# Performance work log

Hardware: AMD Instinct MI355X
Metric: run time of the kernel (lower is better)

The kernel has to match this reference:

```python
import jax, jax.numpy as jnp
import numpy as np

BATCH = 4096
DIM = 2048
TEMP = 0.5
EPS = 1e-12  # matches F.normalize eps


def setup_inputs() -> dict:
    key = jax.random.key(0)
    k1, k2 = jax.random.split(key)
    x_i = jax.random.normal(k1, (BATCH, DIM), dtype=jnp.float32)
    x_j = jax.random.normal(k2, (BATCH, DIM), dtype=jnp.float32)
    return {"x_i": x_i, "x_j": x_j}


def _l2_normalize(x):
    # F.normalize(x, dim=1): x / max(||x||, eps)
    n = jnp.sqrt(jnp.sum(x * x, axis=1, keepdims=True))
    return x / jnp.maximum(n, EPS)


def reference(x_i, x_j):
    N = x_i.shape[0]
    z = jnp.concatenate([_l2_normalize(x_i), _l2_normalize(x_j)], axis=0)  # (2N, D)
    # cosine sim of unit vectors == dot product -> single GEMM instead of (2N,2N,D) broadcast
    sim = z @ z.T  # (2N, 2N)
    # positives: diag offset +N and -N
    sim_ij = jnp.diagonal(sim, offset=N)
    sim_ji = jnp.diagonal(sim, offset=-N)
    pos = jnp.concatenate([sim_ij, sim_ji], axis=0)  # (2N,)
    nom = jnp.exp(pos / TEMP)
    neg_mask = 1.0 - jnp.eye(2 * N, dtype=sim.dtype)
    denom = jnp.sum(neg_mask * jnp.exp(sim / TEMP), axis=1)  # (2N,)
    return jnp.sum(-jnp.log(nom / denom)) / (2 * N)
```

## Files before the change

### kernel.cpp

```cpp
#include <hip/hip_runtime.h>
#include <hip/hip_bf16.h>

#define N_ROWS 8192
#define N_HALF 4096
#define DIM    2048
#define ROWB   2048
#define INV_T  2.0f
#define QSCL   64.0f
#define SIMSCL 0.00048828125f
#define NG1    1024
#define NG2    256
#define NKT    32

typedef __attribute__((ext_vector_type(4))) float f32x4;
typedef __attribute__((ext_vector_type(2))) long lx2;

__device__ __forceinline__ void gload_lds16(const void* g, void* l) {
  __builtin_amdgcn_global_load_lds(
      (const __attribute__((address_space(1))) unsigned int*)g,
      (__attribute__((address_space(3))) unsigned int*)l, 16, 0, 0);
}

__global__ __launch_bounds__(256) void normpos_k(
    const float* __restrict__ xi, const float* __restrict__ xj,
    char* __restrict__ zq, float* __restrict__ pos,
    float* __restrict__ selfd, float* __restrict__ denom)
{
  const int b = blockIdx.x;
  const int t = threadIdx.x;
  const float4* si = (const float4*)(xi + (size_t)b * DIM);
  const float4* sj = (const float4*)(xj + (size_t)b * DIM);
  float4 a0 = si[t * 2], a1 = si[t * 2 + 1];
  float4 c0 = sj[t * 2], c1 = sj[t * 2 + 1];
  float ssi = a0.x*a0.x + a0.y*a0.y + a0.z*a0.z + a0.w*a0.w
            + a1.x*a1.x + a1.y*a1.y + a1.z*a1.z + a1.w*a1.w;
  float ssj = c0.x*c0.x + c0.y*c0.y + c0.z*c0.z + c0.w*c0.w
            + c1.x*c1.x + c1.y*c1.y + c1.z*c1.z + c1.w*c1.w;
  #pragma unroll
  for (int m = 1; m < 64; m <<= 1) {
    ssi += __shfl_xor(ssi, m, 64);
    ssj += __shfl_xor(ssj, m, 64);
  }
  __shared__ float ri[4], rj[4];
  if ((t & 63) == 0) { ri[t >> 6] = ssi; rj[t >> 6] = ssj; }
  __syncthreads();
  float sci = 1.0f / fmaxf(sqrtf(ri[0] + ri[1] + ri[2] + ri[3]), 1e-12f);
  float scj = 1.0f / fmaxf(sqrtf(rj[0] + rj[1] + rj[2] + rj[3]), 1e-12f);

  float fi[8] = {a0.x, a0.y, a0.z, a0.w, a1.x, a1.y, a1.z, a1.w};
  float fj[8] = {c0.x, c0.y, c0.z, c0.w, c1.x, c1.y, c1.z, c1.w};
  float ni[8], nj[8];
  float dp = 0.f;
  #pragma unroll
  for (int e = 0; e < 8; ++e) {
    ni[e] = fi[e] * sci;
    nj[e] = fj[e] * scj;
    dp += ni[e] * nj[e];
  }
  int wi0 = 0, wi1 = 0, wj0 = 0, wj1 = 0;
  wi0 = __builtin_amdgcn_cvt_pk_fp8_f32(ni[0]*QSCL, ni[1]*QSCL, wi0, false);
  wi0 = __builtin_amdgcn_cvt_pk_fp8_f32(ni[2]*QSCL, ni[3]*QSCL, wi0, true);
  wi1 = __builtin_amdgcn_cvt_pk_fp8_f32(ni[4]*QSCL, ni[5]*QSCL, wi1, false);
  wi1 = __builtin_amdgcn_cvt_pk_fp8_f32(ni[6]*QSCL, ni[7]*QSCL, wi1, true);
  wj0 = __builtin_amdgcn_cvt_pk_fp8_f32(nj[0]*QSCL, nj[1]*QSCL, wj0, false);
  wj0 = __builtin_amdgcn_cvt_pk_fp8_f32(nj[2]*QSCL, nj[3]*QSCL, wj0, true);
  wj1 = __builtin_amdgcn_cvt_pk_fp8_f32(nj[4]*QSCL, nj[5]*QSCL, wj1, false);
  wj1 = __builtin_amdgcn_cvt_pk_fp8_f32(nj[6]*QSCL, nj[7]*QSCL, wj1, true);

  const size_t ipos = (size_t)(t >> 3) * 64 + (t & 3) * 16 + ((t >> 2) & 1) * 8;
  *(int2*)(zq + (size_t)b * ROWB + ipos)            = make_int2(wi0, wi1);
  *(int2*)(zq + (size_t)(b + N_HALF) * ROWB + ipos) = make_int2(wj0, wj1);

  float dsi = 0.f, dsj = 0.f;
  {
    float d;
    d = __builtin_amdgcn_cvt_f32_fp8(wi0, 0); dsi += d * d;
    d = __builtin_amdgcn_cvt_f32_fp8(wi0, 1); dsi += d * d;
    d = __builtin_amdgcn_cvt_f32_fp8(wi0, 2); dsi += d * d;
    d = __builtin_amdgcn_cvt_f32_fp8(wi0, 3); dsi += d * d;
    d = __builtin_amdgcn_cvt_f32_fp8(wi1, 0); dsi += d * d;
    d = __builtin_amdgcn_cvt_f32_fp8(wi1, 1); dsi += d * d;
    d = __builtin_amdgcn_cvt_f32_fp8(wi1, 2); dsi += d * d;
    d = __builtin_amdgcn_cvt_f32_fp8(wi1, 3); dsi += d * d;
    d = __builtin_amdgcn_cvt_f32_fp8(wj0, 0); dsj += d * d;
    d = __builtin_amdgcn_cvt_f32_fp8(wj0, 1); dsj += d * d;
    d = __builtin_amdgcn_cvt_f32_fp8(wj0, 2); dsj += d * d;
    d = __builtin_amdgcn_cvt_f32_fp8(wj0, 3); dsj += d * d;
    d = __builtin_amdgcn_cvt_f32_fp8(wj1, 0); dsj += d * d;
    d = __builtin_amdgcn_cvt_f32_fp8(wj1, 1); dsj += d * d;
    d = __builtin_amdgcn_cvt_f32_fp8(wj1, 2); dsj += d * d;
    d = __builtin_amdgcn_cvt_f32_fp8(wj1, 3); dsj += d * d;
  }
  #pragma unroll
  for (int m = 1; m < 64; m <<= 1) {
    dp  += __shfl_xor(dp, m, 64);
    dsi += __shfl_xor(dsi, m, 64);
    dsj += __shfl_xor(dsj, m, 64);
  }
  __shared__ float rp[4], rsi[4], rsj[4];
  if ((t & 63) == 0) { rp[t >> 6] = dp; rsi[t >> 6] = dsi; rsj[t >> 6] = dsj; }
  __syncthreads();
  if (t == 0) {
    float p = rp[0] + rp[1] + rp[2] + rp[3];
    pos[b]            = p;
    pos[b + N_HALF]   = p;
    selfd[b]          = rsi[0] + rsi[1] + rsi[2] + rsi[3];
    selfd[b + N_HALF] = rsj[0] + rsj[1] + rsj[2] + rsj[3];
    denom[b]          = 0.f;
    denom[b + N_HALF] = 0.f;
  }
}

__global__ __launch_bounds__(512, 4) void simexp_k(
    const char* __restrict__ zq, float* __restrict__ denom)
{
  __shared__ char lds[73728];
  char* ldsA = lds;
  char* ldsB = lds + 49152;

  const int t    = threadIdx.x;
  const int wave = t >> 6, lane = t & 63;
  const int o    = lane >> 4;
  const int bid  = blockIdx.x;

  const int sqq = t >> 3;
  const int s0  = (t & 7) ^ (sqq & 7);
  const int srr = s0 >> 2;
  const int so  = s0 & 3;

  if (bid < NG1) {
    const int wr = wave >> 1, wc = wave & 1;

    int rem = (bid & 7) * (NG1 / 8) + (bid >> 3);
    int bi = 0;
    while (rem >= 63 - 2 * bi) { rem -= 63 - 2 * bi; ++bi; }
    const int bj   = 2 * bi + rem;
    const int row0 = bi * 256;
    const int col0 = bj * 128;

    const char* srcA0 = zq + (size_t)(row0 + 2 * sqq + srr) * ROWB + so * 16;
    const char* srcA1 = srcA0 + (size_t)128 * ROWB;
    const char* srcB  = zq + (size_t)(col0 + 2 * sqq + srr) * ROWB + so * 16;
    char* dA = ldsA + wave * 1024;
    char* dB = ldsB + wave * 1024;

    int offA[4], offB[4];
    #pragma unroll
    for (int m = 0; m < 4; ++m) {
      int r = wr * 64 + m * 16 + (lane & 15);
      int q = r >> 1;
      offA[m] = q * 128 + ((((r & 1) * 4 + o) ^ (q & 7)) << 4);
    }
    #pragma unroll
    for (int n = 0; n < 4; ++n) {
      int r = wc * 64 + n * 16 + (lane & 15);
      int q = r >> 1;
      offB[n] = q * 128 + ((((r & 1) * 4 + o) ^ (q & 7)) << 4);
    }

    f32x4 acc[4][4] = {};

#define STAGE(kt, slot) do {                                   \
      gload_lds16(srcA0 + (kt) * 64, dA + (slot) * 16384);     \
      gload_lds16(srcA1 + (kt) * 64, dA + (slot) * 16384 + 8192); \
      gload_lds16(srcB  + (kt) * 64, dB + (slot) * 8192);      \
    } while (0)

    STAGE(0, 0);
    STAGE(1, 1);

    int sl = 0;
    for (int p = 0; p < NKT; ++p) {
      if (p < NKT - 1) asm volatile("s_waitcnt vmcnt(3)" ::: "memory");
      else             asm volatile("s_waitcnt vmcnt(0)" ::: "memory");
      __builtin_amdgcn_s_barrier();
      __builtin_amdgcn_sched_barrier(0);

      const char* Ab = ldsA + sl * 16384;
      const char* Bb = ldsB + sl * 8192;
      lx2 a[4], b[4];
      #pragma unroll
      for (int m = 0; m < 4; ++m) a[m] = *(const lx2*)(Ab + offA[m]);
      #pragma unroll
      for (int n = 0; n < 4; ++n) b[n] = *(const lx2*)(Bb + offB[n]);

      if (p + 2 < NKT) {
        int s2 = sl + 2; if (s2 >= 3) s2 -= 3;
        STAGE(p + 2, s2);
      }

      __builtin_amdgcn_s_setprio(1);
      #pragma unroll
      for (int m = 0; m < 4; ++m)
        #pragma unroll
        for (int n = 0; n < 4; ++n)
          acc[m][n] = __builtin_amdgcn_mfma_f32_16x16x32_fp8_fp8(
              a[m][0], b[n][0], acc[m][n], 0, 0, 0);
      #pragma unroll
      for (int m = 0; m < 4; ++m)
        #pragma unroll
        for (int n = 0; n < 4; ++n)
          acc[m][n] = __builtin_amdgcn_mfma_f32_16x16x32_fp8_fp8(
              a[m][1], b[n][1], acc[m][n], 0, 0, 0);
      __builtin_amdgcn_s_setprio(0);
      __builtin_amdgcn_sched_barrier(0);

      if (++sl >= 3) sl = 0;
    }
#undef STAGE

    #pragma unroll
    for (int m = 0; m < 4; ++m)
      #pragma unroll
      for (int n = 0; n < 4; ++n)
        #pragma unroll
        for (int r = 0; r < 4; ++r)
          acc[m][n][r] = __expf(acc[m][n][r] * SIMSCL);

    #pragma unroll
    for (int m = 0; m < 4; ++m) {
      #pragma unroll
      for (int r = 0; r < 4; ++r) {
        float s = acc[m][0][r] + acc[m][1][r] + acc[m][2][r] + acc[m][3][r];
        s += __shfl_xor(s, 1, 64);
        s += __shfl_xor(s, 2, 64);
        s += __shfl_xor(s, 4, 64);
        s += __shfl_xor(s, 8, 64);
        if ((lane & 15) == 0) {
          int grow = row0 + wr * 64 + m * 16 + (lane >> 4) * 4 + r;
          atomicAdd(&denom[grow], s);
        }
      }
    }

    if (bj >= 2 * bi + 2) {
      #pragma unroll
      for (int n = 0; n < 4; ++n) {
        float cs = 0.f;
        #pragma unroll
        for (int m = 0; m < 4; ++m)
          #pragma unroll
          for (int r = 0; r < 4; ++r)
            cs += acc[m][n][r];
        cs += __shfl_xor(cs, 16, 64);
        cs += __shfl_xor(cs, 32, 64);
        if ((lane >> 4) == 0) {
          int gcol = col0 + wc * 64 + n * 16 + (lane & 15);
          atomicAdd(&denom[gcol], cs);
        }
      }
    }
  } else {
    const int sub  = bid - NG1;
    const int bi   = sub >> 3;
    const int row0 = bi * 256 + (sub & 7) * 32;
    const int col0 = 8064;

    const char* srcB = zq + (size_t)(col0 + 2 * sqq + srr) * ROWB + so * 16;
    const int tA   = t & 127;
    const int sqA  = tA >> 3;
    const int s0A  = (tA & 7) ^ (sqA & 7);
    const char* srcAs = zq + (size_t)(row0 + 2 * sqA + (s0A >> 2)) * ROWB
                      + (s0A & 3) * 16;

    int offA2[2], offB0;
    #pragma unroll
    for (int m = 0; m < 2; ++m) {
      int r = m * 16 + (lane & 15);
      int q = r >> 1;
      offA2[m] = q * 128 + ((((r & 1) * 4 + o) ^ (q & 7)) << 4);
    }
    {
      int r = wave * 16 + (lane & 15);
      int q = r >> 1;
      offB0 = q * 128 + ((((r & 1) * 4 + o) ^ (q & 7)) << 4);
    }

    f32x4 acc2[2] = {};

#define STAGE_T(kt, slot) do {                                            \
      gload_lds16(srcB + (kt) * 64, ldsB + (slot) * 8192 + wave * 1024);  \
      if (wave < 2)                                                       \
        gload_lds16(srcAs + (kt) * 64,                                    \
                    ldsA + (slot) * 2048 + wave * 1024);                  \
    } while (0)

    STAGE_T(0, 0);
    STAGE_T(1, 1);

    int sl = 0;
    for (int p = 0; p < NKT; ++p) {
      if (p < NKT - 1) {
        if (wave < 2) asm volatile("s_waitcnt vmcnt(2)" ::: "memory");
        else          asm volatile("s_waitcnt vmcnt(1)" ::: "memory");
      } else {
        asm volatile("s_waitcnt vmcnt(0)" ::: "memory");
      }
      __builtin_amdgcn_s_barrier();
      __builtin_amdgcn_sched_barrier(0);

      const char* Ab = ldsA + sl * 2048;
      const char* Bb = ldsB + sl * 8192;
      lx2 a0 = *(const lx2*)(Ab + offA2[0]);
      lx2 a1 = *(const lx2*)(Ab + offA2[1]);
      lx2 b0 = *(const lx2*)(Bb + offB0);

      if (p + 2 < NKT) {
        int s2 = sl + 2; if (s2 >= 3) s2 -= 3;
        STAGE_T(p + 2, s2);
      }

      __builtin_amdgcn_s_setprio(1);
      acc2[0] = __builtin_amdgcn_mfma_f32_16x16x32_fp8_fp8(a0[0], b0[0], acc2[0], 0, 0, 0);
      acc2[1] = __builtin_amdgcn_mfma_f32_16x16x32_fp8_fp8(a1[0], b0[0], acc2[1], 0, 0, 0);
      acc2[0] = __builtin_amdgcn_mfma_f32_16x16x32_fp8_fp8(a0[1], b0[1], acc2[0], 0, 0, 0);
      acc2[1] = __builtin_amdgcn_mfma_f32_16x16x32_fp8_fp8(a1[1], b0[1], acc2[1], 0, 0, 0);
      __builtin_amdgcn_s_setprio(0);
      __builtin_amdgcn_sched_barrier(0);

      if (++sl >= 3) sl = 0;
    }
#undef STAGE_T

    #pragma unroll
    for (int m = 0; m < 2; ++m)
      #pragma unroll
      for (int r = 0; r < 4; ++r)
        acc2[m][r] = __expf(acc2[m][r] * SIMSCL);

    #pragma unroll
    for (int m = 0; m < 2; ++m) {
      #pragma unroll
      for (int r = 0; r < 4; ++r) {
        float s = acc2[m][r];
        s += __shfl_xor(s, 1, 64);
        s += __shfl_xor(s, 2, 64);
        s += __shfl_xor(s, 4, 64);
        s += __shfl_xor(s, 8, 64);
        if ((lane & 15) == 0) {
          int grow = row0 + m * 16 + (lane >> 4) * 4 + r;
          atomicAdd(&denom[grow], s);
        }
      }
    }

    if (bi <= 30) {
      float cs = 0.f;
      #pragma unroll
      for (int m = 0; m < 2; ++m)
        #pragma unroll
        for (int r = 0; r < 4; ++r)
          cs += acc2[m][r];
      cs += __shfl_xor(cs, 16, 64);
      cs += __shfl_xor(cs, 32, 64);
      if ((lane >> 4) == 0) {
        int gcol = col0 + wave * 16 + (lane & 15);
        atomicAdd(&denom[gcol], cs);
      }
    }
  }
}

__global__ __launch_bounds__(256) void loss_k(
    const float* __restrict__ denom, const float* __restrict__ pos,
    const float* __restrict__ selfd, float* __restrict__ out)
{
  const int t = threadIdx.x;
  float acc = 0.f;
  for (int i = t; i < N_ROWS; i += 256) {
    float d = denom[i] - __expf(selfd[i] * SIMSCL);
    acc += __logf(d) - pos[i] * INV_T;
  }
  #pragma unroll
  for (int m = 1; m < 64; m <<= 1) acc += __shfl_xor(acc, m, 64);
  __shared__ float red[4];
  if ((t & 63) == 0) red[t >> 6] = acc;
  __syncthreads();
  if (t == 0) out[0] = (red[0] + red[1] + red[2] + red[3]) / (float)N_ROWS;
}

extern "C" void kernel_launch(void* const* d_in, const int* in_sizes, int n_in,
                              void* d_out, int out_size, void* d_ws, size_t ws_size,
                              hipStream_t stream) {
  const float* xi = (const float*)d_in[0];
  const float* xj = (const float*)d_in[1];
  float* out = (float*)d_out;

  char*  ws    = (char*)d_ws;
  char*  zq    = ws;
  float* denom = (float*)(ws + (size_t)N_ROWS * ROWB);
  float* pos   = denom + N_ROWS;
  float* selfd = pos + N_ROWS;

  normpos_k<<<N_HALF, 256, 0, stream>>>(xi, xj, zq, pos, selfd, denom);
  simexp_k<<<NG1 + NG2, 512, 0, stream>>>(zq, denom);
  loss_k<<<1, 256, 0, stream>>>(denom, pos, selfd, out);
}
```

Measured before the change: 124.8 us.

## Switch FP8 GEMM to 32x32x64 scaled MFMA with new fragment layout

Replaces the 16x16x32 fp8 MFMA tiles with the gfx950 scaled 32x32x64 f8f6f4 MFMA using unit scales, so each wave issues fewer, larger matrix instructions per K-step. The LDS fragment offsets, the accumulator layout and the row/column reduction mapping are reworked to match the 32x32 output layout. The tail blocks are regrouped to 64-row tiles, halving their count. The normalize kernel now writes fp8 rows in plain order instead of the previous interleaved permutation to match the new operand layout. This risks precision or layout mismatch and higher register pressure from the 16-wide accumulators.

Measured after the change: 136.9 us. 1.1x slower.

```diff
diff --git a/kernel.cpp b/kernel.cpp
--- a/kernel.cpp
+++ b/kernel.cpp
@@ -8,12 +8,15 @@
 #define INV_T  2.0f
 #define QSCL   64.0f
 #define SIMSCL 0.00048828125f
+#define SCONE  0x7F7F7F7F
 #define NG1    1024
-#define NG2    256
+#define NG2    128
 #define NKT    32
 
-typedef __attribute__((ext_vector_type(4))) float f32x4;
-typedef __attribute__((ext_vector_type(2))) long lx2;
+typedef __attribute__((ext_vector_type(4)))  float f32x4;
+typedef __attribute__((ext_vector_type(16))) float f32x16;
+typedef __attribute__((ext_vector_type(4)))  int   i32x4;
+typedef __attribute__((ext_vector_type(8)))  int   i32x8;
 
 __device__ __forceinline__ void gload_lds16(const void* g, void* l) {
   __builtin_amdgcn_global_load_lds(
@@ -66,10 +69,8 @@
   wj0 = __builtin_amdgcn_cvt_pk_fp8_f32(nj[2]*QSCL, nj[3]*QSCL, wj0, true);
   wj1 = __builtin_amdgcn_cvt_pk_fp8_f32(nj[4]*QSCL, nj[5]*QSCL, wj1, false);
   wj1 = __builtin_amdgcn_cvt_pk_fp8_f32(nj[6]*QSCL, nj[7]*QSCL, wj1, true);
-
-  const size_t ipos = (size_t)(t >> 3) * 64 + (t & 3) * 16 + ((t >> 2) & 1) * 8;
-  *(int2*)(zq + (size_t)b * ROWB + ipos)            = make_int2(wi0, wi1);
-  *(int2*)(zq + (size_t)(b + N_HALF) * ROWB + ipos) = make_int2(wj0, wj1);
+  ((int2*)(zq + (size_t)b * ROWB))[t]            = make_int2(wi0, wi1);
+  ((int2*)(zq + (size_t)(b + N_HALF) * ROWB))[t] = make_int2(wj0, wj1);
 
   float dsi = 0.f, dsj = 0.f;
   {
@@ -120,7 +121,7 @@
 
   const int t    = threadIdx.x;
   const int wave = t >> 6, lane = t & 63;
-  const int o    = lane >> 4;
+  const int h    = lane >> 5;
   const int bid  = blockIdx.x;
 
   const int sqq = t >> 3;
@@ -144,21 +145,25 @@
     char* dA = ldsA + wave * 1024;
     char* dB = ldsB + wave * 1024;
 
-    int offA[4], offB[4];
-    #pragma unroll
-    for (int m = 0; m < 4; ++m) {
-      int r = wr * 64 + m * 16 + (lane & 15);
-      int q = r >> 1;
-      offA[m] = q * 128 + ((((r & 1) * 4 + o) ^ (q & 7)) << 4);
-    }
-    #pragma unroll
-    for (int n = 0; n < 4; ++n) {
-      int r = wc * 64 + n * 16 + (lane & 15);
-      int q = r >> 1;
-      offB[n] = q * 128 + ((((r & 1) * 4 + o) ^ (q & 7)) << 4);
-    }
-
-    f32x4 acc[4][4] = {};
+    int offA[2][2], offB[2][2];
+    #pragma unroll
+    for (int m = 0; m < 2; ++m)
+      #pragma unroll
+      for (int j = 0; j < 2; ++j) {
+        int r = wr * 64 + m * 32 + (lane & 31);
+        int q = r >> 1, c = h * 2 + j;
+        offA[m][j] = q * 128 + ((((r & 1) * 4 + c) ^ (q & 7)) << 4);
+      }
+    #pragma unroll
+    for (int n = 0; n < 2; ++n)
+      #pragma unroll
+      for (int j = 0; j < 2; ++j) {
+        int r = wc * 64 + n * 32 + (lane & 31);
+        int q = r >> 1, c = h * 2 + j;
+        offB[n][j] = q * 128 + ((((r & 1) * 4 + c) ^ (q & 7)) << 4);
+      }
+
+    f32x16 acc[2][2] = {};
 
 #define STAGE(kt, slot) do {                                   \
       gload_lds16(srcA0 + (kt) * 64, dA + (slot) * 16384);     \
@@ -178,11 +183,19 @@
 
       const char* Ab = ldsA + sl * 16384;
       const char* Bb = ldsB + sl * 8192;
-      lx2 a[4], b[4];
-      #pragma unroll
-      for (int m = 0; m < 4; ++m) a[m] = *(const lx2*)(Ab + offA[m]);
-      #pragma unroll
-      for (int n = 0; n < 4; ++n) b[n] = *(const lx2*)(Bb + offB[n]);
+      i32x8 a[2], b[2];
+      #pragma unroll
+      for (int m = 0; m < 2; ++m) {
+        i32x4 lo = *(const i32x4*)(Ab + offA[m][0]);
+        i32x4 hi = *(const i32x4*)(Ab + offA[m][1]);
+        a[m] = __builtin_shufflevector(lo, hi, 0, 1, 2, 3, 4, 5, 6, 7);
+      }
+      #pragma unroll
+      for (int n = 0; n < 2; ++n) {
+        i32x4 lo = *(const i32x4*)(Bb + offB[n][0]);
+        i32x4 hi = *(const i32x4*)(Bb + offB[n][1]);
+        b[n] = __builtin_shufflevector(lo, hi, 0, 1, 2, 3, 4, 5, 6, 7);
+      }
 
       if (p + 2 < NKT) {
         int s2 = sl + 2; if (s2 >= 3) s2 -= 3;
@@ -191,17 +204,11 @@
 
       __builtin_amdgcn_s_setprio(1);
       #pragma unroll
-      for (int m = 0; m < 4; ++m)
+      for (int m = 0; m < 2; ++m)
         #pragma unroll
-        for (int n = 0; n < 4; ++n)
-          acc[m][n] = __builtin_amdgcn_mfma_f32_16x16x32_fp8_fp8(
-              a[m][0], b[n][0], acc[m][n], 0, 0, 0);
-      #pragma unroll
-      for (int m = 0; m < 4; ++m)
-        #pragma unroll
-        for (int n = 0; n < 4; ++n)
-          acc[m][n] = __builtin_amdgcn_mfma_f32_16x16x32_fp8_fp8(
-              a[m][1], b[n][1], acc[m][n], 0, 0, 0);
+        for (int n = 0; n < 2; ++n)
+          acc[m][n] = __builtin_amdgcn_mfma_scale_f32_32x32x64_f8f6f4(
+              a[m], b[n], acc[m][n], 0, 0, 0, SCONE, 0, SCONE);
       __builtin_amdgcn_s_setprio(0);
       __builtin_amdgcn_sched_barrier(0);
 
@@ -210,24 +217,25 @@
 #undef STAGE
 
     #pragma unroll
-    for (int m = 0; m < 4; ++m)
-      #pragma unroll
-      for (int n = 0; n < 4; ++n)
+    for (int m = 0; m < 2; ++m)
+      #pragma unroll
+      for (int n = 0; n < 2; ++n)
         #pragma unroll
-        for (int r = 0; r < 4; ++r)
+        for (int r = 0; r < 16; ++r)
           acc[m][n][r] = __expf(acc[m][n][r] * SIMSCL);
 
     #pragma unroll
-    for (int m = 0; m < 4; ++m) {
-      #pragma unroll
-      for (int r = 0; r < 4; ++r) {
-        float s = acc[m][0][r] + acc[m][1][r] + acc[m][2][r] + acc[m][3][r];
+    for (int m = 0; m < 2; ++m) {
+      #pragma unroll
+      for (int r = 0; r < 16; ++r) {
+        float s = acc[m][0][r] + acc[m][1][r];
         s += __shfl_xor(s, 1, 64);
         s += __shfl_xor(s, 2, 64);
         s += __shfl_xor(s, 4, 64);
         s += __shfl_xor(s, 8, 64);
-        if ((lane & 15) == 0) {
-          int grow = row0 + wr * 64 + m * 16 + (lane >> 4) * 4 + r;
+        s += __shfl_xor(s, 16, 64);
+        if ((lane & 31) == 0) {
+          int grow = row0 + wr * 64 + m * 32 + (r & 3) + 8 * (r >> 2) + 4 * h;
           atomicAdd(&denom[grow], s);
         }
       }
@@ -235,54 +243,55 @@
 
     if (bj >= 2 * bi + 2) {
       #pragma unroll
-      for (int n = 0; n < 4; ++n) {
+      for (int n = 0; n < 2; ++n) {
         float cs = 0.f;
         #pragma unroll
-        for (int m = 0; m < 4; ++m)
+        for (int m = 0; m < 2; ++m)
           #pragma unroll
-          for (int r = 0; r < 4; ++r)
+          for (int r = 0; r < 16; ++r)
             cs += acc[m][n][r];
-        cs += __shfl_xor(cs, 16, 64);
         cs += __shfl_xor(cs, 32, 64);
-        if ((lane >> 4) == 0) {
-          int gcol = col0 + wc * 64 + n * 16 + (lane & 15);
+        if (lane < 32) {
+          int gcol = col0 + wc * 64 + n * 32 + lane;
           atomicAdd(&denom[gcol], cs);
         }
       }
     }
   } else {
     const int sub  = bid - NG1;
-    const int bi   = sub >> 3;
-    const int row0 = bi * 256 + (sub & 7) * 32;
+    const int bi   = sub >> 2;
+    const int row0 = bi * 256 + (sub & 3) * 64;
     const int col0 = 8064;
+    const int wr   = wave >> 2, wc = wave & 3;
 
     const char* srcB = zq + (size_t)(col0 + 2 * sqq + srr) * ROWB + so * 16;
-    const int tA   = t & 127;
+    const int tA   = t & 255;
     const int sqA  = tA >> 3;
     const int s0A  = (tA & 7) ^ (sqA & 7);
     const char* srcAs = zq + (size_t)(row0 + 2 * sqA + (s0A >> 2)) * ROWB
                       + (s0A & 3) * 16;
 
-    int offA2[2], offB0;
-    #pragma unroll
-    for (int m = 0; m < 2; ++m) {
-      int r = m * 16 + (lane & 15);
-      int q = r >> 1;
-      offA2[m] = q * 128 + ((((r & 1) * 4 + o) ^ (q & 7)) << 4);
-    }
-    {
-      int r = wave * 16 + (lane & 15);
-      int q = r >> 1;
-      offB0 = q * 128 + ((((r & 1) * 4 + o) ^ (q & 7)) << 4);
-    }
-
-    f32x4 acc2[2] = {};
+    int offA2[2], offB2[2];
+    #pragma unroll
+    for (int j = 0; j < 2; ++j) {
+      int r = wr * 32 + (lane & 31);
+      int q = r >> 1, c = h * 2 + j;
+      offA2[j] = q * 128 + ((((r & 1) * 4 + c) ^ (q & 7)) << 4);
+    }
+    #pragma unroll
+    for (int j = 0; j < 2; ++j) {
+      int r = wc * 32 + (lane & 31);
+      int q = r >> 1, c = h * 2 + j;
+      offB2[j] = q * 128 + ((((r & 1) * 4 + c) ^ (q & 7)) << 4);
+    }
+
+    f32x16 acc2 = {};
 
 #define STAGE_T(kt, slot) do {                                            \
       gload_lds16(srcB + (kt) * 64, ldsB + (slot) * 8192 + wave * 1024);  \
-      if (wave < 2)                                                       \
+      if (wave < 4)                                                       \
         gload_lds16(srcAs + (kt) * 64,                                    \
-                    ldsA + (slot) * 2048 + wave * 1024);                  \
+                    ldsA + (slot) * 4096 + wave * 1024);                  \
     } while (0)
 
     STAGE_T(0, 0);
@@ -291,7 +300,7 @@
     int sl = 0;
     for (int p = 0; p < NKT; ++p) {
       if (p < NKT - 1) {
-        if (wave < 2) asm volatile("s_waitcnt vmcnt(2)" ::: "memory");
+        if (wave < 4) asm volatile("s_waitcnt vmcnt(2)" ::: "memory");
         else          asm volatile("s_waitcnt vmcnt(1)" ::: "memory");
       } else {
         asm volatile("s_waitcnt vmcnt(0)" ::: "memory");
@@ -299,11 +308,14 @@
       __builtin_amdgcn_s_barrier();
       __builtin_amdgcn_sched_barrier(0);
 
-      const char* Ab = ldsA + sl * 2048;
+      const char* Ab = ldsA + sl * 4096;
       const char* Bb = ldsB + sl * 8192;
-      lx2 a0 = *(const lx2*)(Ab + offA2[0]);
-      lx2 a1 = *(const lx2*)(Ab + offA2[1]);
-      lx2 b0 = *(const lx2*)(Bb + offB0);
+      i32x4 alo = *(const i32x4*)(Ab + offA2[0]);
+      i32x4 ahi = *(const i32x4*)(Ab + offA2[1]);
+      i32x4 blo = *(const i32x4*)(Bb + offB2[0]);
+      i32x4 bhi = *(const i32x4*)(Bb + offB2[1]);
+      i32x8 a = __builtin_shufflevector(alo, ahi, 0, 1, 2, 3, 4, 5, 6, 7);
+      i32x8 b = __builtin_shufflevector(blo, bhi, 0, 1, 2, 3, 4, 5, 6, 7);
 
       if (p + 2 < NKT) {
         int s2 = sl + 2; if (s2 >= 3) s2 -= 3;
@@ -311,10 +323,8 @@
       }
 
       __builtin_amdgcn_s_setprio(1);
-      acc2[0] = __builtin_amdgcn_mfma_f32_16x16x32_fp8_fp8(a0[0], b0[0], acc2[0], 0, 0, 0);
-      acc2[1] = __builtin_amdgcn_mfma_f32_16x16x32_fp8_fp8(a1[0], b0[0], acc2[1], 0, 0, 0);
-      acc2[0] = __builtin_amdgcn_mfma_f32_16x16x32_fp8_fp8(a0[1], b0[1], acc2[0], 0, 0, 0);
-      acc2[1] = __builtin_amdgcn_mfma_f32_16x16x32_fp8_fp8(a1[1], b0[1], acc2[1], 0, 0, 0);
+      acc2 = __builtin_amdgcn_mfma_scale_f32_32x32x64_f8f6f4(
+          a, b, acc2, 0, 0, 0, SCONE, 0, SCONE);
       __builtin_amdgcn_s_setprio(0);
       __builtin_amdgcn_sched_barrier(0);
 
@@ -323,38 +333,30 @@
 #undef STAGE_T
 
     #pragma unroll
-    for (int m = 0; m < 2; ++m)
-      #pragma unroll
-      for (int r = 0; r < 4; ++r)
-        acc2[m][r] = __expf(acc2[m][r] * SIMSCL);
-
-    #pragma unroll
-    for (int m = 0; m < 2; ++m) {
-      #pragma unroll
-      for (int r = 0; r < 4; ++r) {
-        float s = acc2[m][r];
-        s += __shfl_xor(s, 1, 64);
-        s += __shfl_xor(s, 2, 64);
-        s += __shfl_xor(s, 4, 64);
-        s += __shfl_xor(s, 8, 64);
-        if ((lane & 15) == 0) {
-          int grow = row0 + m * 16 + (lane >> 4) * 4 + r;
-          atomicAdd(&denom[grow], s);
-        }
+    for (int r = 0; r < 16; ++r)
+      acc2[r] = __expf(acc2[r] * SIMSCL);
+
+    #pragma unroll
+    for (int r = 0; r < 16; ++r) {
+      float s = acc2[r];
+      s += __shfl_xor(s, 1, 64);
+      s += __shfl_xor(s, 2, 64);
+      s += __shfl_xor(s, 4, 64);
+      s += __shfl_xor(s, 8, 64);
+      s += __shfl_xor(s, 16, 64);
+      if ((lane & 31) == 0) {
+        int grow = row0 + wr * 32 + (r & 3) + 8 * (r >> 2) + 4 * h;
+        atomicAdd(&denom[grow], s);
       }
     }
 
     if (bi <= 30) {
       float cs = 0.f;
       #pragma unroll
-      for (int m = 0; m < 2; ++m)
-        #pragma unroll
-        for (int r = 0; r < 4; ++r)
-          cs += acc2[m][r];
-      cs += __shfl_xor(cs, 16, 64);
+      for (int r = 0; r < 16; ++r) cs += acc2[r];
       cs += __shfl_xor(cs, 32, 64);
-      if ((lane >> 4) == 0) {
-        int gcol = col0 + wave * 16 + (lane & 15);
+      if (lane < 32) {
+        int gcol = col0 + wc * 32 + lane;
         atomicAdd(&denom[gcol], cs);
       }
     }
```

## Halve simexp block to 256 threads with 128x64 per-wave tiles

Applied to the files above, without the earlier changes.

The similarity/exp kernel now runs 4 waves per block instead of 8, and each wave computes twice as many output tiles (8x4 MFMA accumulators instead of 4x4; 2x2 in the tail path). Each thread issues more global-to-LDS loads per stage, and the vmcnt waits are adjusted to match. This raises register-level reuse of LDS fragments per MFMA and cuts LDS read traffic per FLOP. The cost is higher VGPR pressure from 128 accumulator floats and fewer waves available to hide latency.

Result: slower. 128.2 us (+2.7%).

```diff
diff --git a/kernel.cpp b/kernel.cpp
--- a/kernel.cpp
+++ b/kernel.cpp
@@ -111,7 +111,7 @@
   }
 }
 
-__global__ __launch_bounds__(512, 4) void simexp_k(
+__global__ __launch_bounds__(256, 2) void simexp_k(
     const char* __restrict__ zq, float* __restrict__ denom)
 {
   __shared__ char lds[73728];
@@ -138,16 +138,15 @@
     const int row0 = bi * 256;
     const int col0 = bj * 128;
 
-    const char* srcA0 = zq + (size_t)(row0 + 2 * sqq + srr) * ROWB + so * 16;
-    const char* srcA1 = srcA0 + (size_t)128 * ROWB;
-    const char* srcB  = zq + (size_t)(col0 + 2 * sqq + srr) * ROWB + so * 16;
+    const char* srcA = zq + (size_t)(row0 + 2 * sqq + srr) * ROWB + so * 16;
+    const char* srcB = zq + (size_t)(col0 + 2 * sqq + srr) * ROWB + so * 16;
     char* dA = ldsA + wave * 1024;
     char* dB = ldsB + wave * 1024;
 
-    int offA[4], offB[4];
-    #pragma unroll
-    for (int m = 0; m < 4; ++m) {
-      int r = wr * 64 + m * 16 + (lane & 15);
+    int offA[8], offB[4];
+    #pragma unroll
+    for (int m = 0; m < 8; ++m) {
+      int r = wr * 128 + m * 16 + (lane & 15);
       int q = r >> 1;
       offA[m] = q * 128 + ((((r & 1) * 4 + o) ^ (q & 7)) << 4);
     }
@@ -158,12 +157,15 @@
       offB[n] = q * 128 + ((((r & 1) * 4 + o) ^ (q & 7)) << 4);
     }
 
-    f32x4 acc[4][4] = {};
-
-#define STAGE(kt, slot) do {                                   \
-      gload_lds16(srcA0 + (kt) * 64, dA + (slot) * 16384);     \
-      gload_lds16(srcA1 + (kt) * 64, dA + (slot) * 16384 + 8192); \
-      gload_lds16(srcB  + (kt) * 64, dB + (slot) * 8192);      \
+    f32x4 acc[8][4] = {};
+
+#define STAGE(kt, slot) do {                                              \
+      gload_lds16(srcA + (kt) * 64,                        dA + (slot) * 16384);          \
+      gload_lds16(srcA + (kt) * 64 + (size_t) 64 * ROWB,   dA + (slot) * 16384 + 4096);   \
+      gload_lds16(srcA + (kt) * 64 + (size_t)128 * ROWB,   dA + (slot) * 16384 + 8192);   \
+      gload_lds16(srcA + (kt) * 64 + (size_t)192 * ROWB,   dA + (slot) * 16384 + 12288);  \
+      gload_lds16(srcB + (kt) * 64,                        dB + (slot) * 8192);           \
+      gload_lds16(srcB + (kt) * 64 + (size_t) 64 * ROWB,   dB + (slot) * 8192 + 4096);    \
     } while (0)
 
     STAGE(0, 0);
@@ -171,16 +173,16 @@
 
     int sl = 0;
     for (int p = 0; p < NKT; ++p) {
-      if (p < NKT - 1) asm volatile("s_waitcnt vmcnt(3)" ::: "memory");
+      if (p < NKT - 1) asm volatile("s_waitcnt vmcnt(6)" ::: "memory");
       else             asm volatile("s_waitcnt vmcnt(0)" ::: "memory");
       __builtin_amdgcn_s_barrier();
       __builtin_amdgcn_sched_barrier(0);
 
       const char* Ab = ldsA + sl * 16384;
       const char* Bb = ldsB + sl * 8192;
-      lx2 a[4], b[4];
-      #pragma unroll
-      for (int m = 0; m < 4; ++m) a[m] = *(const lx2*)(Ab + offA[m]);
+      lx2 a[8], b[4];
+      #pragma unroll
+      for (int m = 0; m < 8; ++m) a[m] = *(const lx2*)(Ab + offA[m]);
       #pragma unroll
       for (int n = 0; n < 4; ++n) b[n] = *(const lx2*)(Bb + offB[n]);
 
@@ -191,13 +193,13 @@
 
       __builtin_amdgcn_s_setprio(1);
       #pragma unroll
-      for (int m = 0; m < 4; ++m)
+      for (int m = 0; m < 8; ++m)
         #pragma unroll
         for (int n = 0; n < 4; ++n)
           acc[m][n] = __builtin_amdgcn_mfma_f32_16x16x32_fp8_fp8(
               a[m][0], b[n][0], acc[m][n], 0, 0, 0);
       #pragma unroll
-      for (int m = 0; m < 4; ++m)
+      for (int m = 0; m < 8; ++m)
         #pragma unroll
         for (int n = 0; n < 4; ++n)
           acc[m][n] = __builtin_amdgcn_mfma_f32_16x16x32_fp8_fp8(
@@ -210,7 +212,7 @@
 #undef STAGE
 
     #pragma unroll
-    for (int m = 0; m < 4; ++m)
+    for (int m = 0; m < 8; ++m)
       #pragma unroll
       for (int n = 0; n < 4; ++n)
         #pragma unroll
@@ -218,7 +220,7 @@
           acc[m][n][r] = __expf(acc[m][n][r] * SIMSCL);
 
     #pragma unroll
-    for (int m = 0; m < 4; ++m) {
+    for (int m = 0; m < 8; ++m) {
       #pragma unroll
       for (int r = 0; r < 4; ++r) {
         float s = acc[m][0][r] + acc[m][1][r] + acc[m][2][r] + acc[m][3][r];
@@ -227,7 +229,7 @@
         s += __shfl_xor(s, 4, 64);
         s += __shfl_xor(s, 8, 64);
         if ((lane & 15) == 0) {
-          int grow = row0 + wr * 64 + m * 16 + (lane >> 4) * 4 + r;
+          int grow = row0 + wr * 128 + m * 16 + (lane >> 4) * 4 + r;
           atomicAdd(&denom[grow], s);
         }
       }
@@ -238,7 +240,7 @@
       for (int n = 0; n < 4; ++n) {
         float cs = 0.f;
         #pragma unroll
-        for (int m = 0; m < 4; ++m)
+        for (int m = 0; m < 8; ++m)
           #pragma unroll
           for (int r = 0; r < 4; ++r)
             cs += acc[m][n][r];
@@ -263,23 +265,25 @@
     const char* srcAs = zq + (size_t)(row0 + 2 * sqA + (s0A >> 2)) * ROWB
                       + (s0A & 3) * 16;
 
-    int offA2[2], offB0;
+    int offA2[2], offB2[2];
     #pragma unroll
     for (int m = 0; m < 2; ++m) {
       int r = m * 16 + (lane & 15);
       int q = r >> 1;
       offA2[m] = q * 128 + ((((r & 1) * 4 + o) ^ (q & 7)) << 4);
     }
-    {
-      int r = wave * 16 + (lane & 15);
+    #pragma unroll
+    for (int n = 0; n < 2; ++n) {
+      int r = wave * 32 + n * 16 + (lane & 15);
       int q = r >> 1;
-      offB0 = q * 128 + ((((r & 1) * 4 + o) ^ (q & 7)) << 4);
-    }
-
-    f32x4 acc2[2] = {};
+      offB2[n] = q * 128 + ((((r & 1) * 4 + o) ^ (q & 7)) << 4);
+    }
+
+    f32x4 acc2[2][2] = {};
 
 #define STAGE_T(kt, slot) do {                                            \
-      gload_lds16(srcB + (kt) * 64, ldsB + (slot) * 8192 + wave * 1024);  \
+      gload_lds16(srcB + (kt) * 64,                      ldsB + (slot) * 8192 + wave * 1024);        \
+      gload_lds16(srcB + (kt) * 64 + (size_t)64 * ROWB,  ldsB + (slot) * 8192 + 4096 + wave * 1024); \
       if (wave < 2)                                                       \
         gload_lds16(srcAs + (kt) * 64,                                    \
                     ldsA + (slot) * 2048 + wave * 1024);                  \
@@ -291,8 +295,8 @@
     int sl = 0;
     for (int p = 0; p < NKT; ++p) {
       if (p < NKT - 1) {
-        if (wave < 2) asm volatile("s_waitcnt vmcnt(2)" ::: "memory");
-        else          asm volatile("s_waitcnt vmcnt(1)" ::: "memory");
+        if (wave < 2) asm volatile("s_waitcnt vmcnt(3)" ::: "memory");
+        else          asm volatile("s_waitcnt vmcnt(2)" ::: "memory");
       } else {
         asm volatile("s_waitcnt vmcnt(0)" ::: "memory");
       }
@@ -303,7 +307,8 @@
       const char* Bb = ldsB + sl * 8192;
       lx2 a0 = *(const lx2*)(Ab + offA2[0]);
       lx2 a1 = *(const lx2*)(Ab + offA2[1]);
-      lx2 b0 = *(const lx2*)(Bb + offB0);
+      lx2 b0 = *(const lx2*)(Bb + offB2[0]);
+      lx2 b1 = *(const lx2*)(Bb + offB2[1]);
 
       if (p + 2 < NKT) {
         int s2 = sl + 2; if (s2 >= 3) s2 -= 3;
@@ -311,10 +316,14 @@
       }
 
       __builtin_amdgcn_s_setprio(1);
-      acc2[0] = __builtin_amdgcn_mfma_f32_16x16x32_fp8_fp8(a0[0], b0[0], acc2[0], 0, 0, 0);
-      acc2[1] = __builtin_amdgcn_mfma_f32_16x16x32_fp8_fp8(a1[0], b0[0], acc2[1], 0, 0, 0);
-      acc2[0] = __builtin_amdgcn_mfma_f32_16x16x32_fp8_fp8(a0[1], b0[1], acc2[0], 0, 0, 0);
-      acc2[1] = __builtin_amdgcn_mfma_f32_16x16x32_fp8_fp8(a1[1], b0[1], acc2[1], 0, 0, 0);
+      acc2[0][0] = __builtin_amdgcn_mfma_f32_16x16x32_fp8_fp8(a0[0], b0[0], acc2[0][0], 0, 0, 0);
+      acc2[0][1] = __builtin_amdgcn_mfma_f32_16x16x32_fp8_fp8(a0[0], b1[0], acc2[0][1], 0, 0, 0);
+      acc2[1][0] = __builtin_amdgcn_mfma_f32_16x16x32_fp8_fp8(a1[0], b0[0], acc2[1][0], 0, 0, 0);
+      acc2[1][1] = __builtin_amdgcn_mfma_f32_16x16x32_fp8_fp8(a1[0], b1[0], acc2[1][1], 0, 0, 0);
+      acc2[0][0] = __builtin_amdgcn_mfma_f32_16x16x32_fp8_fp8(a0[1], b0[1], acc2[0][0], 0, 0, 0);
+      acc2[0][1] = __builtin_amdgcn_mfma_f32_16x16x32_fp8_fp8(a0[1], b1[1], acc2[0][1], 0, 0, 0);
+      acc2[1][0] = __builtin_amdgcn_mfma_f32_16x16x32_fp8_fp8(a1[1], b0[1], acc2[1][0], 0, 0, 0);
+      acc2[1][1] = __builtin_amdgcn_mfma_f32_16x16x32_fp8_fp8(a1[1], b1[1], acc2[1][1], 0, 0, 0);
       __builtin_amdgcn_s_setprio(0);
       __builtin_amdgcn_sched_barrier(0);
 
@@ -325,14 +334,16 @@
     #pragma unroll
     for (int m = 0; m < 2; ++m)
       #pragma unroll
-      for (int r = 0; r < 4; ++r)
-        acc2[m][r] = __expf(acc2[m][r] * SIMSCL);
+      for (int n = 0; n < 2; ++n)
+        #pragma unroll
+        for (int r = 0; r < 4; ++r)
+          acc2[m][n][r] = __expf(acc2[m][n][r] * SIMSCL);
 
     #pragma unroll
     for (int m = 0; m < 2; ++m) {
       #pragma unroll
       for (int r = 0; r < 4; ++r) {
-        float s = acc2[m][r];
+        float s = acc2[m][0][r] + acc2[m][1][r];
         s += __shfl_xor(s, 1, 64);
         s += __shfl_xor(s, 2, 64);
         s += __shfl_xor(s, 4, 64);
@@ -345,17 +356,20 @@
     }
 
     if (bi <= 30) {
-      float cs = 0.f;
-      #pragma unroll
-      for (int m = 0; m < 2; ++m)
-        #pragma unroll
-        for (int r = 0; r < 4; ++r)
-          cs += acc2[m][r];
-      cs += __shfl_xor(cs, 16, 64);
-      cs += __shfl_xor(cs, 32, 64);
-      if ((lane >> 4) == 0) {
-        int gcol = col0 + wave * 16 + (lane & 15);
-        atomicAdd(&denom[gcol], cs);
+      #pragma unroll
+      for (int n = 0; n < 2; ++n) {
+        float cs = 0.f;
+        #pragma unroll
+        for (int m = 0; m < 2; ++m)
+          #pragma unroll
+          for (int r = 0; r < 4; ++r)
+            cs += acc2[m][n][r];
+        cs += __shfl_xor(cs, 16, 64);
+        cs += __shfl_xor(cs, 32, 64);
+        if ((lane >> 4) == 0) {
+          int gcol = col0 + wave * 32 + n * 16 + (lane & 15);
+          atomicAdd(&denom[gcol], cs);
+        }
       }
     }
   }
@@ -393,6 +407,6 @@
   float* selfd = pos + N_ROWS;
 
   normpos_k<<<N_HALF, 256, 0, stream>>>(xi, xj, zq, pos, selfd, denom);
-  simexp_k<<<NG1 + NG2, 512, 0, stream>>>(zq, denom);
+  simexp_k<<<NG1 + NG2, 256, 0, stream>>>(zq, denom);
   loss_k<<<1, 256, 0, stream>>>(denom, pos, selfd, out);
 }
```
